# Optimization experiments

Hardware: AMD Instinct MI355X
Metric: run time of the kernel (lower is better)

The kernel has to match this reference:

```python
import jax, jax.numpy as jnp
import numpy as np

# hyperparams (match init_kwargs)
B, T, DV, DJ, L = 32, 256, 1024, 512, 20
K, S, LAYERS = 4, 2, 3
LAM = 4.0            # lambda_softmax used inside frame_by_word attention
MARGIN = 0.1         # opt.global_margin
EPS_BN = 1e-5
EPS_COS = 1e-8


def _bn(x):
    # training-mode BatchNorm1d(affine=False): per-channel stats over (batch, length)
    m = x.mean(axis=(0, 2), keepdims=True)
    v = ((x - m) ** 2).mean(axis=(0, 2), keepdims=True)
    return (x - m) / jnp.sqrt(v + EPS_BN)


def _conv1d(x, w, b, stride):
    # x: [N, Cin, L], w: [Cout, Cin, K], padding=0
    y = jax.lax.conv_general_dilated(x, w, (stride,), 'VALID',
                                     dimension_numbers=('NCH', 'OIH', 'NCH'))
    return y + b[None, :, None]


def setup_inputs() -> dict:
    key = jax.random.key(0)
    ks = jax.random.split(key, 10)
    inp = {
        'video': jax.random.normal(ks[0], (B, T, DV), jnp.float32),
        'words': jax.random.normal(ks[1], (B, L, DJ), jnp.float32),
        'w_masks': jnp.ones((B, L), jnp.float32),
        'conv0_w': jax.random.normal(ks[2], (DJ, DV, K), jnp.float32) * 0.02,
        'conv0_b': jnp.zeros((DJ,), jnp.float32),
        'conv1_w': jax.random.normal(ks[3], (DJ, DJ, K), jnp.float32) * 0.02,
        'conv1_b': jnp.zeros((DJ,), jnp.float32),
        'conv2_w': jax.random.normal(ks[4], (DJ, DJ, K), jnp.float32) * 0.02,
        'conv2_b': jnp.zeros((DJ,), jnp.float32),
        'conv1d_w': jax.random.normal(ks[5], (DJ, DJ, 1), jnp.float32) * 0.02,
        'conv1d_b': jnp.zeros((DJ,), jnp.float32),
    }
    return inp


def reference(video, words, w_masks, conv0_w, conv0_b, conv1_w, conv1_b,
              conv2_w, conv2_b, conv1d_w, conv1d_b):
    # --- conv/batchnorm feature extraction ---
    x = _bn(video.transpose(0, 2, 1))                     # [b, DV, T]
    feats = []
    for w_, b_ in ((conv0_w, conv0_b), (conv1_w, conv1_b), (conv2_w, conv2_b)):
        x = jax.nn.relu(_conv1d(x, w_, b_, S))
        feats.append(x)
    v = jnp.concatenate(feats, axis=-1)                   # [b, DJ, T']
    v = _conv1d(v, conv1d_w, conv1d_b, 1)
    v = _bn(v).transpose(0, 2, 1)                         # [b, T', DJ]
    w = _bn(words.transpose(0, 2, 1)).transpose(0, 2, 1)  # [b, L, DJ]

    # --- batched frame-by-word cross-attention over all (sentence i, video j) pairs ---
    att = jnp.einsum('jtd,ild->ijtl', v, w) * LAM         # [b_i, b_j, T', L]
    mask = (w_masks > 0.5)[:, None, None, :]
    att = jax.nn.softmax(jnp.where(mask, att, -1e9), axis=-1)
    v_s = jnp.einsum('ijtl,ild->ijtd', att, w)            # [b_i, b_j, T', DJ]

    # cosine similarity along feature dim
    num = jnp.einsum('jtd,ijtd->ijt', v, v_s)
    vn = jnp.maximum(jnp.linalg.norm(v, axis=-1), EPS_COS)[None]     # [1, b_j, T']
    vsn = jnp.maximum(jnp.linalg.norm(v_s, axis=-1), EPS_COS)        # [b_i, b_j, T']
    sim = num / (vn * vsn)                                # [b_i, b_j, T']

    b = sim.shape[0]
    idx = jnp.arange(b)
    positive_map = sim[idx, idx]                          # [b, T']
    scores = sim.max(axis=-1)                             # [b_i, b_j]

    # --- diag margin ranking loss ---
    dg = jnp.diagonal(scores)
    cost_s = jnp.clip(MARGIN + scores - dg[:, None], 0.0)
    cost_im = jnp.clip(MARGIN + scores - dg[None, :], 0.0)
    I = jnp.eye(b, dtype=bool)
    cost_s = jnp.where(I, 0.0, cost_s)
    cost_im = jnp.where(I, 0.0, cost_im)
    loss = cost_s.sum() / b + cost_im.sum() / b
    return loss, positive_map
```

## Files before the change

### kernel.cpp

```cpp
#include <hip/hip_runtime.h>
#include <math.h>

#define B_   32
#define T_   256
#define DV_  1024
#define DJ_  512
#define L_   20
#define T0_  127
#define T1_  62
#define T2_  30
#define TP_  219
#define LAM_ 4.0f
#define MARGIN_ 0.1f

typedef __attribute__((ext_vector_type(8))) short short8;
typedef __attribute__((ext_vector_type(4))) float f32x4;

static __device__ __forceinline__ unsigned short f2bf(float f) {
  union { float f; unsigned u; } v; v.f = f;
  unsigned r = v.u + 0x7fff + ((v.u >> 16) & 1);
  return (unsigned short)(r >> 16);
}

struct ushort4_t { unsigned short x, y, z, w; };

#define GLOAD_LDS16(gp, lp)                                                      \
  __builtin_amdgcn_global_load_lds(                                              \
      (const __attribute__((address_space(1))) void*)(gp),                       \
      (__attribute__((address_space(3))) void*)(lp), 16, 0, 0)

__global__ void reorder_all_k(const float* __restrict__ c0w, const float* __restrict__ c1w,
                              const float* __restrict__ c2w, const float* __restrict__ pww,
                              unsigned short* __restrict__ W0, unsigned short* __restrict__ W1,
                              unsigned short* __restrict__ W2, unsigned short* __restrict__ Wp) {
  int bid = blockIdx.x;
  if (bid < 2048) {
    int idx = bid * 256 + threadIdx.x;
    int co = idx >> 10, ci = idx & 1023;
    float4 w = *reinterpret_cast<const float4*>(c0w + (size_t)idx * 4);
    unsigned short* d = W0 + (size_t)co * 4096 + ci;
    d[0] = f2bf(w.x); d[1024] = f2bf(w.y); d[2048] = f2bf(w.z); d[3072] = f2bf(w.w);
  } else if (bid < 3072) {
    int idx = (bid - 2048) * 256 + threadIdx.x;
    int co = idx >> 9, ci = idx & 511;
    float4 w = *reinterpret_cast<const float4*>(c1w + (size_t)idx * 4);
    unsigned short* d = W1 + (size_t)co * 2048 + ci;
    d[0] = f2bf(w.x); d[512] = f2bf(w.y); d[1024] = f2bf(w.z); d[1536] = f2bf(w.w);
  } else if (bid < 4096) {
    int idx = (bid - 3072) * 256 + threadIdx.x;
    int co = idx >> 9, ci = idx & 511;
    float4 w = *reinterpret_cast<const float4*>(c2w + (size_t)idx * 4);
    unsigned short* d = W2 + (size_t)co * 2048 + ci;
    d[0] = f2bf(w.x); d[512] = f2bf(w.y); d[1024] = f2bf(w.z); d[1536] = f2bf(w.w);
  } else {
    int idx = (bid - 4096) * 256 + threadIdx.x;
    float4 v = *reinterpret_cast<const float4*>(pww + (size_t)idx * 4);
    ushort4_t h = { f2bf(v.x), f2bf(v.y), f2bf(v.z), f2bf(v.w) };
    reinterpret_cast<ushort4_t*>(Wp)[idx] = h;
  }
}

__global__ void stats1_k(const float* __restrict__ x, float* __restrict__ part,
                         int C, int rows, int rpg, int cpgShift) {
  int cpg  = 1 << cpgShift;
  int c4   = threadIdx.x & (cpg - 1);
  int rsub = threadIdx.x >> cpgShift;
  int nsub = 256 >> cpgShift;
  int r0 = blockIdx.x * rpg + rsub;
  int r1 = min(blockIdx.x * rpg + rpg, rows);
  float4 s = {0.f,0.f,0.f,0.f}, q = {0.f,0.f,0.f,0.f};
  for (int r = r0; r < r1; r += nsub) {
    float4 v = *reinterpret_cast<const float4*>(&x[(size_t)r * C + c4 * 4]);
    s.x += v.x; s.y += v.y; s.z += v.z; s.w += v.w;
    q.x += v.x*v.x; q.y += v.y*v.y; q.z += v.z*v.z; q.w += v.w*v.w;
  }
  float* ps = part + ((size_t)blockIdx.x * nsub + rsub) * 2 * C;
  reinterpret_cast<float4*>(ps)[c4] = s;
  reinterpret_cast<float4*>(ps + C)[c4] = q;
}

__global__ void stats2_k(const float* __restrict__ part, float* __restrict__ ms,
                         int C, int ng, float inv_n) {
  __shared__ float4 sS[8][33], sQ[8][33];
  int c4l = threadIdx.x & 31;
  int gs  = threadIdx.x >> 5;
  int c4  = blockIdx.x * 32 + c4l;
  float4 s = {0.f,0.f,0.f,0.f}, q = {0.f,0.f,0.f,0.f};
  for (int g = gs; g < ng; g += 8) {
    const float4* ps = reinterpret_cast<const float4*>(part + (size_t)g * 2 * C);
    float4 a = ps[c4];
    float4 b = ps[(C >> 2) + c4];
    s.x += a.x; s.y += a.y; s.z += a.z; s.w += a.w;
    q.x += b.x; q.y += b.y; q.z += b.z; q.w += b.w;
  }
  sS[gs][c4l] = s; sQ[gs][c4l] = q;
  __syncthreads();
  if (gs == 0) {
    float4 S = sS[0][c4l], Q = sQ[0][c4l];
#pragma unroll
    for (int k = 1; k < 8; ++k) {
      float4 a = sS[k][c4l], b = sQ[k][c4l];
      S.x += a.x; S.y += a.y; S.z += a.z; S.w += a.w;
      Q.x += b.x; Q.y += b.y; Q.z += b.z; Q.w += b.w;
    }
    int c = c4 * 4;
    float m0 = S.x * inv_n, m1 = S.y * inv_n, m2 = S.z * inv_n, m3 = S.w * inv_n;
    ms[c+0] = m0; ms[C+c+0] = rsqrtf(Q.x * inv_n - m0*m0 + 1e-5f);
    ms[c+1] = m1; ms[C+c+1] = rsqrtf(Q.y * inv_n - m1*m1 + 1e-5f);
    ms[c+2] = m2; ms[C+c+2] = rsqrtf(Q.z * inv_n - m2*m2 + 1e-5f);
    ms[c+3] = m3; ms[C+c+3] = rsqrtf(Q.w * inv_n - m3*m3 + 1e-5f);
  }
}

__global__ void vid_bn_cast_k(const float* __restrict__ video,
                              const float* __restrict__ ms,
                              unsigned short* __restrict__ vbf) {
  int i4 = blockIdx.x * 256 + threadIdx.x;
  float4 v = reinterpret_cast<const float4*>(video)[i4];
  int c = (i4 & 255) * 4;
  v.x = (v.x - ms[c+0]) * ms[1024+c+0];
  v.y = (v.y - ms[c+1]) * ms[1024+c+1];
  v.z = (v.z - ms[c+2]) * ms[1024+c+2];
  v.w = (v.w - ms[c+3]) * ms[1024+c+3];
  ushort4_t h = { f2bf(v.x), f2bf(v.y), f2bf(v.z), f2bf(v.w) };
  reinterpret_cast<ushort4_t*>(vbf)[i4] = h;
}

template<bool RELU, bool BIAS, bool OUT_BF16, bool PARTIAL>
__global__ __launch_bounds__(256) void mfma_gemm_k(
    const unsigned short* __restrict__ xin, const unsigned short* __restrict__ Wr,
    const float* __restrict__ bias, void* __restrict__ out,
    int b_stride, int row_off, int row_t_stride,
    int To, int M, int t_off_out, int ldout, int Ktot, int Kloc)
{
  __shared__ __align__(16) short As[2][128 * 32];
  __shared__ __align__(16) short Bs[2][128 * 32];

  const int tid  = threadIdx.x;
  const int lane = tid & 63;
  const int wv   = tid >> 6;
  const int wr   = wv >> 1;
  const int wc   = wv & 1;
  const int mbase = blockIdx.x * 128;
  const int nbase = blockIdx.y * 128;
  const int kstart = PARTIAL ? blockIdx.z * Kloc : 0;

  const int srow = tid >> 2;
  const int sb   = (((tid & 3) ^ ((srow ^ (srow >> 2)) & 3))) * 8;
  int ma0 = min(mbase + srow,      M - 1);
  int ma1 = min(mbase + 64 + srow, M - 1);
  int ba0 = ma0 / To, ta0 = ma0 % To;
  int ba1 = ma1 / To, ta1 = ma1 % To;
  const unsigned short* agp0 = xin + (size_t)ba0 * b_stride + row_off
                               + (size_t)ta0 * row_t_stride + sb + kstart;
  const unsigned short* agp1 = xin + (size_t)ba1 * b_stride + row_off
                               + (size_t)ta1 * row_t_stride + sb + kstart;
  const unsigned short* bgp0 = Wr + (size_t)(nbase + srow) * Ktot + sb + kstart;
  const unsigned short* bgp1 = Wr + (size_t)(nbase + 64 + srow) * Ktot + sb + kstart;

  f32x4 acc[4][4] = {};
  const int nsteps = Kloc >> 5;

#define STAGE(buf, k0)                                        \
  do {                                                        \
    GLOAD_LDS16(agp0 + (k0), &As[buf][wv * 512]);             \
    GLOAD_LDS16(agp1 + (k0), &As[buf][2048 + wv * 512]);      \
    GLOAD_LDS16(bgp0 + (k0), &Bs[buf][wv * 512]);             \
    GLOAD_LDS16(bgp1 + (k0), &Bs[buf][2048 + wv * 512]);      \
  } while (0)

  STAGE(0, 0);
  __syncthreads();

  const int l15   = lane & 15;
  const int rsw   = (l15 ^ (l15 >> 2)) & 3;
  const int chunk = ((lane >> 4) ^ rsw) * 8;
  const int a_off = (wr * 64 + l15) * 32 + chunk;
  const int b_off = (wc * 64 + l15) * 32 + chunk;

  for (int s = 0; s < nsteps; ++s) {
    const int nb = s & 1;
    if (s + 1 < nsteps) STAGE(nb ^ 1, (s + 1) * 32);

    const short* Ab = &As[nb][a_off];
    const short* Bb = &Bs[nb][b_off];
    short8 af[4], bf[4];
#pragma unroll
    for (int f = 0; f < 4; ++f) {
      af[f] = *reinterpret_cast<const short8*>(Ab + f * 512);
      bf[f] = *reinterpret_cast<const short8*>(Bb + f * 512);
    }
#pragma unroll
    for (int fm = 0; fm < 4; ++fm)
#pragma unroll
      for (int fn = 0; fn < 4; ++fn)
        acc[fm][fn] = __builtin_amdgcn_mfma_f32_16x16x32_bf16(af[fm], bf[fn], acc[fm][fn], 0, 0, 0);

    __syncthreads();
  }
#undef STAGE

  const int cl = lane & 15, rh = lane >> 4;
#pragma unroll
  for (int fm = 0; fm < 4; ++fm) {
#pragma unroll
    for (int fn = 0; fn < 4; ++fn) {
      int col = nbase + wc * 64 + fn * 16 + cl;
      float bv = BIAS ? bias[col] : 0.f;
      f32x4 v = acc[fm][fn];
#pragma unroll
      for (int r = 0; r < 4; ++r) {
        int m = mbase + wr * 64 + fm * 16 + rh * 4 + r;
        if (m < M) {
          if (PARTIAL) {
            float* pout = (float*)out + (size_t)blockIdx.z * ((size_t)M * ldout);
            pout[(size_t)m * ldout + col] = v[r];
          } else {
            int b = m / To, to = m % To;
            float x = v[r] + bv;
            if (RELU) x = fmaxf(x, 0.f);
            size_t oi = ((size_t)b * TP_ + t_off_out + to) * (size_t)ldout + col;
            if (OUT_BF16) ((unsigned short*)out)[oi] = f2bf(x);
            else          ((float*)out)[oi] = x;
          }
        }
      }
    }
  }
}

template<int S>
__global__ void reduce_conv_k(const float* __restrict__ part, const float* __restrict__ bias,
                              unsigned short* __restrict__ outb,
                              int M, int To, int t_off_out) {
  int idx = blockIdx.x * 256 + threadIdx.x;
  int m = idx >> 7, n4 = idx & 127;
  if (m >= M) return;
  size_t off = (size_t)m * 512 + n4 * 4;
  float4 a = *reinterpret_cast<const float4*>(part + off);
#pragma unroll
  for (int s = 1; s < S; ++s) {
    float4 b = *reinterpret_cast<const float4*>(part + (size_t)s * M * 512 + off);
    a.x += b.x; a.y += b.y; a.z += b.z; a.w += b.w;
  }
  float4 bv = *reinterpret_cast<const float4*>(bias + n4 * 4);
  a.x = fmaxf(a.x + bv.x, 0.f);
  a.y = fmaxf(a.y + bv.y, 0.f);
  a.z = fmaxf(a.z + bv.z, 0.f);
  a.w = fmaxf(a.w + bv.w, 0.f);
  int b_ = m / To, to = m % To;
  ushort4_t h = { f2bf(a.x), f2bf(a.y), f2bf(a.z), f2bf(a.w) };
  reinterpret_cast<ushort4_t*>(outb + ((size_t)b_ * TP_ + t_off_out + to) * 512)[n4] = h;
}

__global__ void v2_norm_vn_k(float* __restrict__ v2, const float* __restrict__ ms,
                             unsigned short* __restrict__ v2bf, float* __restrict__ vn) {
  int r = blockIdx.x, t = threadIdx.x;
  float* row = v2 + (size_t)r * DJ_;
  unsigned short* brow = v2bf + (size_t)r * DJ_;
  float ss = 0.f;
#pragma unroll
  for (int h = 0; h < 2; ++h) {
    int c4 = t + h * 64;
    float4 v = reinterpret_cast<float4*>(row)[c4];
    int c = c4 * 4;
    v.x = (v.x - ms[c+0]) * ms[DJ_+c+0];
    v.y = (v.y - ms[c+1]) * ms[DJ_+c+1];
    v.z = (v.z - ms[c+2]) * ms[DJ_+c+2];
    v.w = (v.w - ms[c+3]) * ms[DJ_+c+3];
    reinterpret_cast<float4*>(row)[c4] = v;
    ushort4_t h4 = { f2bf(v.x), f2bf(v.y), f2bf(v.z), f2bf(v.w) };
    reinterpret_cast<ushort4_t*>(brow)[c4] = h4;
    ss += v.x*v.x + v.y*v.y + v.z*v.z + v.w*v.w;
  }
#pragma unroll
  for (int o = 32; o; o >>= 1) ss += __shfl_down(ss, o, 64);
  if (t == 0) vn[r] = sqrtf(ss);
}

__global__ void wnorm_k(const float* __restrict__ words, const float* __restrict__ ms,
                        float* __restrict__ wbn, unsigned short* __restrict__ wbnb) {
  int idx = blockIdx.x * 256 + threadIdx.x;
  if (idx >= (B_ * L_ * DJ_) / 4) return;
  int c = (idx & 127) * 4;
  float4 v = reinterpret_cast<const float4*>(words)[idx];
  v.x = (v.x - ms[c+0]) * ms[DJ_+c+0];
  v.y = (v.y - ms[c+1]) * ms[DJ_+c+1];
  v.z = (v.z - ms[c+2]) * ms[DJ_+c+2];
  v.w = (v.w - ms[c+3]) * ms[DJ_+c+3];
  reinterpret_cast<float4*>(wbn)[idx] = v;
  ushort4_t h = { f2bf(v.x), f2bf(v.y), f2bf(v.z), f2bf(v.w) };
  reinterpret_cast<ushort4_t*>(wbnb)[idx] = h;
}

__global__ void gram_k(const float* __restrict__ wbn, float* __restrict__ G) {
  __shared__ float sw[L_ * 516];
  int i = blockIdx.x, tid = threadIdx.x;
  for (int idx = tid; idx < L_ * DJ_; idx += 256) {
    int l = idx >> 9, d = idx & 511;
    sw[l * 516 + d] = wbn[(size_t)i * L_ * DJ_ + idx];
  }
  __syncthreads();
  for (int p = tid; p < L_ * L_; p += 256) {
    int l = p / L_, l2 = p % L_;
    const float4* a = reinterpret_cast<const float4*>(&sw[l * 516]);
    const float4* b = reinterpret_cast<const float4*>(&sw[l2 * 516]);
    float acc = 0.f;
    for (int d4 = 0; d4 < 128; ++d4) {
      float4 av = a[d4], bv = b[d4];
      acc += av.x*bv.x + av.y*bv.y + av.z*bv.z + av.w*bv.w;
    }
    G[i * 400 + p] = acc;
  }
}

__global__ __launch_bounds__(256) void sim_k(
    const float* __restrict__ A, const float* __restrict__ G,
    const float* __restrict__ vn, const float* __restrict__ wmask,
    float* __restrict__ pos, float* __restrict__ scores) {
  int j = blockIdx.x, i = blockIdx.y;
  __shared__ float sG[400];
  __shared__ float sm[20];
  __shared__ float red[4];
  int tid = threadIdx.x;
  for (int p = tid; p < 400; p += 256) sG[p] = G[i * 400 + p];
  if (tid < 20) sm[tid] = wmask[i * 20 + tid];
  __syncthreads();

  float simv = -1e30f;
  if (tid < TP_) {
    const float* ar = A + ((size_t)j * TP_ + tid) * 640 + i * 20;
    float a[20], p[20];
    float mx = -1e30f;
#pragma unroll
    for (int l = 0; l < 20; ++l) {
      a[l] = ar[l];
      float lg = (sm[l] > 0.5f) ? LAM_ * a[l] : -1e9f;
      p[l] = lg;
      mx = fmaxf(mx, lg);
    }
    float Z = 0.f;
#pragma unroll
    for (int l = 0; l < 20; ++l) { p[l] = __expf(p[l] - mx); Z += p[l]; }
    float invZ = 1.f / Z, num = 0.f;
#pragma unroll
    for (int l = 0; l < 20; ++l) { p[l] *= invZ; num += p[l] * a[l]; }
    float q2 = 0.f;
#pragma unroll
    for (int l = 0; l < 20; ++l) {
      float gi = 0.f;
#pragma unroll
      for (int l2 = 0; l2 < 20; ++l2) gi += sG[l * 20 + l2] * p[l2];
      q2 += p[l] * gi;
    }
    float vnv = fmaxf(vn[(size_t)j * TP_ + tid], 1e-8f);
    float vsnv = fmaxf(sqrtf(q2), 1e-8f);
    simv = num / (vnv * vsnv);
    if (i == j) pos[i * TP_ + tid] = simv;
  }
  float mv = simv;
#pragma unroll
  for (int o = 32; o; o >>= 1) mv = fmaxf(mv, __shfl_down(mv, o, 64));
  if ((tid & 63) == 0) red[tid >> 6] = mv;
  __syncthreads();
  if (tid == 0)
    scores[i * 32 + j] = fmaxf(fmaxf(red[0], red[1]), fmaxf(red[2], red[3]));
}

__global__ void loss_k(const float* __restrict__ scores, float* __restrict__ out) {
  __shared__ float red[16];
  int tid = threadIdx.x;
  int i = tid >> 5, j = tid & 31;
  float s = scores[tid];
  float dgi = scores[i * 32 + i], dgj = scores[j * 32 + j];
  float c = 0.f;
  if (i != j)
    c = fmaxf(0.f, MARGIN_ + s - dgi) + fmaxf(0.f, MARGIN_ + s - dgj);
#pragma unroll
  for (int o = 32; o; o >>= 1) c += __shfl_down(c, o, 64);
  if ((tid & 63) == 0) red[tid >> 6] = c;
  __syncthreads();
  if (tid == 0) {
    float t = 0.f;
    for (int w = 0; w < 16; ++w) t += red[w];
    out[0] = t / 32.f;
  }
}

extern "C" void kernel_launch(void* const* d_in, const int* in_sizes, int n_in,
                              void* d_out, int out_size, void* d_ws, size_t ws_size,
                              hipStream_t stream) {
  const float* video = (const float*)d_in[0];
  const float* words = (const float*)d_in[1];
  const float* wmask = (const float*)d_in[2];
  const float* c0w = (const float*)d_in[3];
  const float* c0b = (const float*)d_in[4];
  const float* c1w = (const float*)d_in[5];
  const float* c1b = (const float*)d_in[6];
  const float* c2w = (const float*)d_in[7];
  const float* c2b = (const float*)d_in[8];
  const float* pww = (const float*)d_in[9];
  const float* pwb = (const float*)d_in[10];
  float* out = (float*)d_out;
  float* ws  = (float*)d_ws;

  float*          W0r    = ws;
  float*          W1r    = W0r + 1048576;
  float*          W2r    = W1r + 524288;
  float*          Wpw    = W2r + 524288;
  float*          AMvbf  = Wpw + 131072;
  float*          vcatb  = AMvbf + 4485120;
  float*          Pbuf   = vcatb + 1794048;
  float*          v2     = Pbuf;
  float*          v2bfp  = v2 + 3588096;
  float*          wbn    = v2bfp + 1794048;
  float*          wbnbp  = wbn + 327680;
  float*          G      = wbnbp + 163840;
  float*          vn     = G + 12800;
  float*          scores = vn + 7008;
  float*          vpart  = scores + 1024;
  float*          vms    = vpart + 1048576;
  float*          v2part = vms + 2048;
  float*          v2ms   = v2part + 897024;
  float*          wpart  = v2ms + 1024;
  float*          wms    = wpart + 81920;

  unsigned short* W0     = (unsigned short*)W0r;
  unsigned short* W1     = (unsigned short*)W1r;
  unsigned short* W2     = (unsigned short*)W2r;
  unsigned short* Wp     = (unsigned short*)Wpw;
  unsigned short* vbf    = (unsigned short*)AMvbf;
  float*          Amat   = AMvbf;
  unsigned short* vcb    = (unsigned short*)vcatb;
  unsigned short* v2bf   = (unsigned short*)v2bfp;
  unsigned short* wbnb   = (unsigned short*)wbnbp;

  reorder_all_k<<<4352, 256, 0, stream>>>(c0w, c1w, c2w, pww, W0, W1, W2, Wp);

  stats1_k<<<512, 256, 0, stream>>>(video, vpart, 1024, 8192, 16, 8);
  stats2_k<<<8, 256, 0, stream>>>(vpart, vms, 1024, 512, 1.f / 8192.f);
  vid_bn_cast_k<<<8192, 256, 0, stream>>>(video, vms, vbf);

  mfma_gemm_k<false, false, false, true><<<dim3(32, 4, 4), 256, 0, stream>>>(
      vbf, W0, nullptr, Pbuf, 262144, 0, 2048, T0_, 32 * T0_, 0, 512, 4096, 1024);
  reduce_conv_k<4><<<2032, 256, 0, stream>>>(Pbuf, c0b, vcb, 32 * T0_, T0_, 0);
  mfma_gemm_k<false, false, false, true><<<dim3(16, 4, 8), 256, 0, stream>>>(
      vcb, W1, nullptr, Pbuf, 112128, 0, 1024, T1_, 32 * T1_, 0, 512, 2048, 256);
  reduce_conv_k<8><<<992, 256, 0, stream>>>(Pbuf, c1b, vcb, 32 * T1_, T1_, T0_);
  mfma_gemm_k<false, false, false, true><<<dim3(8, 4, 8), 256, 0, stream>>>(
      vcb, W2, nullptr, Pbuf, 112128, 65024, 1024, T2_, 32 * T2_, 0, 512, 2048, 256);
  reduce_conv_k<8><<<480, 256, 0, stream>>>(Pbuf, c2b, vcb, 32 * T2_, T2_, T0_ + T1_);

  mfma_gemm_k<false, true, false, false><<<dim3(55, 4), 256, 0, stream>>>(
      vcb, Wp, pwb, v2, 112128, 0, 512, TP_, 32 * TP_, 0, 512, 512, 512);

  stats1_k<<<438, 256, 0, stream>>>(v2, v2part, 512, 7008, 16, 7);
  stats2_k<<<4, 256, 0, stream>>>(v2part, v2ms, 512, 876, 1.f / 7008.f);
  v2_norm_vn_k<<<7008, 64, 0, stream>>>(v2, v2ms, v2bf, vn);

  stats1_k<<<40, 256, 0, stream>>>(words, wpart, 512, 640, 16, 7);
  stats2_k<<<4, 256, 0, stream>>>(wpart, wms, 512, 80, 1.f / 640.f);
  wnorm_k<<<(81920 + 255) / 256, 256, 0, stream>>>(words, wms, wbn, wbnb);
  gram_k<<<32, 256, 0, stream>>>(wbn, G);

  mfma_gemm_k<false, false, false, false><<<dim3(55, 5), 256, 0, stream>>>(
      v2bf, wbnb, nullptr, Amat, 112128, 0, 512, TP_, 32 * TP_, 0, 640, 512, 512);

  sim_k<<<dim3(32, 32), 256, 0, stream>>>(Amat, G, vn, wmask, out + 1, scores);
  loss_k<<<1, 1024, 0, stream>>>(scores, out);
}
```

Before: 246.5 us.

## Template GEMM tile sizes and remap workgroups across XCDs

Turns the MFMA GEMM into a template over the block tile (BM, BN). The conv and projection GEMMs now launch with smaller 64x128 or 64x64 tiles, giving more workgroups to fill the 256 CUs. It also adds a linear workgroup remapping so consecutive tiles land on the same XCD, aiming to improve L2 reuse. Smaller tiles lower per-block arithmetic intensity and raise global and LDS traffic per FLOP.

```diff
diff --git a/kernel.cpp b/kernel.cpp
--- a/kernel.cpp
+++ b/kernel.cpp
@@ -126,47 +126,64 @@
   reinterpret_cast<ushort4_t*>(vbf)[i4] = h;
 }
 
-template<bool RELU, bool BIAS, bool OUT_BF16, bool PARTIAL>
-__global__ __launch_bounds__(256) void mfma_gemm_k(
+template<int BM, int BN, bool RELU, bool BIAS, bool OUT_BF16, bool PARTIAL>
+__global__ __launch_bounds__(256) void gemm_k(
     const unsigned short* __restrict__ xin, const unsigned short* __restrict__ Wr,
     const float* __restrict__ bias, void* __restrict__ out,
     int b_stride, int row_off, int row_t_stride,
     int To, int M, int t_off_out, int ldout, int Ktot, int Kloc)
 {
-  __shared__ __align__(16) short As[2][128 * 32];
-  __shared__ __align__(16) short Bs[2][128 * 32];
+  constexpr int AI = BM / 64, BI = BN / 64;
+  constexpr int FM = BM / 32, FN = BN / 32;
+  __shared__ __align__(16) short As[2][BM * 32];
+  __shared__ __align__(16) short Bs[2][BN * 32];
 
   const int tid  = threadIdx.x;
   const int lane = tid & 63;
   const int wv   = tid >> 6;
   const int wr   = wv >> 1;
   const int wc   = wv & 1;
-  const int mbase = blockIdx.x * 128;
-  const int nbase = blockIdx.y * 128;
-  const int kstart = PARTIAL ? blockIdx.z * Kloc : 0;
+
+  const int gx = gridDim.x, gy = gridDim.y;
+  const int nwg = gx * gy * gridDim.z;
+  const int lin = blockIdx.x + gx * (blockIdx.y + gy * blockIdx.z);
+  const int q = nwg >> 3, r = nwg & 7;
+  const int xcd = lin & 7, sub = lin >> 3;
+  const int work = (xcd < r ? xcd * (q + 1) : r * (q + 1) + (xcd - r) * q) + sub;
+  const int bx = work % gx;
+  const int by = (work / gx) % gy;
+  const int bz = work / (gx * gy);
+
+  const int mbase = bx * BM;
+  const int nbase = by * BN;
+  const int kstart = PARTIAL ? bz * Kloc : 0;
 
   const int srow = tid >> 2;
   const int sb   = (((tid & 3) ^ ((srow ^ (srow >> 2)) & 3))) * 8;
-  int ma0 = min(mbase + srow,      M - 1);
-  int ma1 = min(mbase + 64 + srow, M - 1);
-  int ba0 = ma0 / To, ta0 = ma0 % To;
-  int ba1 = ma1 / To, ta1 = ma1 % To;
-  const unsigned short* agp0 = xin + (size_t)ba0 * b_stride + row_off
-                               + (size_t)ta0 * row_t_stride + sb + kstart;
-  const unsigned short* agp1 = xin + (size_t)ba1 * b_stride + row_off
-                               + (size_t)ta1 * row_t_stride + sb + kstart;
-  const unsigned short* bgp0 = Wr + (size_t)(nbase + srow) * Ktot + sb + kstart;
-  const unsigned short* bgp1 = Wr + (size_t)(nbase + 64 + srow) * Ktot + sb + kstart;
-
-  f32x4 acc[4][4] = {};
+  const unsigned short* agp[AI];
+  const unsigned short* bgp[BI];
+#pragma unroll
+  for (int i = 0; i < AI; ++i) {
+    int ma = min(mbase + i * 64 + srow, M - 1);
+    int b0 = ma / To, t0 = ma % To;
+    agp[i] = xin + (size_t)b0 * b_stride + row_off
+             + (size_t)t0 * row_t_stride + sb + kstart;
+  }
+#pragma unroll
+  for (int i = 0; i < BI; ++i)
+    bgp[i] = Wr + (size_t)(nbase + i * 64 + srow) * Ktot + sb + kstart;
+
+  f32x4 acc[FM][FN] = {};
   const int nsteps = Kloc >> 5;
 
-#define STAGE(buf, k0)                                        \
-  do {                                                        \
-    GLOAD_LDS16(agp0 + (k0), &As[buf][wv * 512]);             \
-    GLOAD_LDS16(agp1 + (k0), &As[buf][2048 + wv * 512]);      \
-    GLOAD_LDS16(bgp0 + (k0), &Bs[buf][wv * 512]);             \
-    GLOAD_LDS16(bgp1 + (k0), &Bs[buf][2048 + wv * 512]);      \
+#define STAGE(buf, k0)                                                \
+  do {                                                                \
+    _Pragma("unroll")                                                 \
+    for (int i = 0; i < AI; ++i)                                      \
+      GLOAD_LDS16(agp[i] + (k0), &As[buf][i * 2048 + wv * 512]);      \
+    _Pragma("unroll")                                                 \
+    for (int i = 0; i < BI; ++i)                                      \
+      GLOAD_LDS16(bgp[i] + (k0), &Bs[buf][i * 2048 + wv * 512]);      \
   } while (0)
 
   STAGE(0, 0);
@@ -175,8 +192,8 @@
   const int l15   = lane & 15;
   const int rsw   = (l15 ^ (l15 >> 2)) & 3;
   const int chunk = ((lane >> 4) ^ rsw) * 8;
-  const int a_off = (wr * 64 + l15) * 32 + chunk;
-  const int b_off = (wc * 64 + l15) * 32 + chunk;
+  const int a_off = (wr * (BM / 2) + l15) * 32 + chunk;
+  const int b_off = (wc * (BN / 2) + l15) * 32 + chunk;
 
   for (int s = 0; s < nsteps; ++s) {
     const int nb = s & 1;
@@ -184,16 +201,17 @@
 
     const short* Ab = &As[nb][a_off];
     const short* Bb = &Bs[nb][b_off];
-    short8 af[4], bf[4];
-#pragma unroll
-    for (int f = 0; f < 4; ++f) {
+    short8 af[FM], bf[FN];
+#pragma unroll
+    for (int f = 0; f < FM; ++f)
       af[f] = *reinterpret_cast<const short8*>(Ab + f * 512);
+#pragma unroll
+    for (int f = 0; f < FN; ++f)
       bf[f] = *reinterpret_cast<const short8*>(Bb + f * 512);
-    }
-#pragma unroll
-    for (int fm = 0; fm < 4; ++fm)
-#pragma unroll
-      for (int fn = 0; fn < 4; ++fn)
+#pragma unroll
+    for (int fm = 0; fm < FM; ++fm)
+#pragma unroll
+      for (int fn = 0; fn < FN; ++fn)
         acc[fm][fn] = __builtin_amdgcn_mfma_f32_16x16x32_bf16(af[fm], bf[fn], acc[fm][fn], 0, 0, 0);
 
     __syncthreads();
@@ -202,22 +220,22 @@
 
   const int cl = lane & 15, rh = lane >> 4;
 #pragma unroll
-  for (int fm = 0; fm < 4; ++fm) {
-#pragma unroll
-    for (int fn = 0; fn < 4; ++fn) {
-      int col = nbase + wc * 64 + fn * 16 + cl;
+  for (int fm = 0; fm < FM; ++fm) {
+#pragma unroll
+    for (int fn = 0; fn < FN; ++fn) {
+      int col = nbase + wc * (BN / 2) + fn * 16 + cl;
       float bv = BIAS ? bias[col] : 0.f;
       f32x4 v = acc[fm][fn];
 #pragma unroll
-      for (int r = 0; r < 4; ++r) {
-        int m = mbase + wr * 64 + fm * 16 + rh * 4 + r;
+      for (int rr = 0; rr < 4; ++rr) {
+        int m = mbase + wr * (BM / 2) + fm * 16 + rh * 4 + rr;
         if (m < M) {
           if (PARTIAL) {
-            float* pout = (float*)out + (size_t)blockIdx.z * ((size_t)M * ldout);
-            pout[(size_t)m * ldout + col] = v[r];
+            float* pout = (float*)out + (size_t)bz * ((size_t)M * ldout);
+            pout[(size_t)m * ldout + col] = v[rr];
           } else {
             int b = m / To, to = m % To;
-            float x = v[r] + bv;
+            float x = v[rr] + bv;
             if (RELU) x = fmaxf(x, 0.f);
             size_t oi = ((size_t)b * TP_ + t_off_out + to) * (size_t)ldout + col;
             if (OUT_BF16) ((unsigned short*)out)[oi] = f2bf(x);
@@ -441,17 +459,17 @@
   stats2_k<<<8, 256, 0, stream>>>(vpart, vms, 1024, 512, 1.f / 8192.f);
   vid_bn_cast_k<<<8192, 256, 0, stream>>>(video, vms, vbf);
 
-  mfma_gemm_k<false, false, false, true><<<dim3(32, 4, 4), 256, 0, stream>>>(
+  gemm_k<64, 128, false, false, false, true><<<dim3(64, 4, 4), 256, 0, stream>>>(
       vbf, W0, nullptr, Pbuf, 262144, 0, 2048, T0_, 32 * T0_, 0, 512, 4096, 1024);
   reduce_conv_k<4><<<2032, 256, 0, stream>>>(Pbuf, c0b, vcb, 32 * T0_, T0_, 0);
-  mfma_gemm_k<false, false, false, true><<<dim3(16, 4, 8), 256, 0, stream>>>(
+  gemm_k<64, 128, false, false, false, true><<<dim3(31, 4, 8), 256, 0, stream>>>(
       vcb, W1, nullptr, Pbuf, 112128, 0, 1024, T1_, 32 * T1_, 0, 512, 2048, 256);
   reduce_conv_k<8><<<992, 256, 0, stream>>>(Pbuf, c1b, vcb, 32 * T1_, T1_, T0_);
-  mfma_gemm_k<false, false, false, true><<<dim3(8, 4, 8), 256, 0, stream>>>(
+  gemm_k<64, 64, false, false, false, true><<<dim3(15, 8, 8), 256, 0, stream>>>(
       vcb, W2, nullptr, Pbuf, 112128, 65024, 1024, T2_, 32 * T2_, 0, 512, 2048, 256);
   reduce_conv_k<8><<<480, 256, 0, stream>>>(Pbuf, c2b, vcb, 32 * T2_, T2_, T0_ + T1_);
 
-  mfma_gemm_k<false, true, false, false><<<dim3(55, 4), 256, 0, stream>>>(
+  gemm_k<64, 64, false, true, false, false><<<dim3(110, 8), 256, 0, stream>>>(
       vcb, Wp, pwb, v2, 112128, 0, 512, TP_, 32 * TP_, 0, 512, 512, 512);
 
   stats1_k<<<438, 256, 0, stream>>>(v2, v2part, 512, 7008, 16, 7);
@@ -463,7 +481,7 @@
   wnorm_k<<<(81920 + 255) / 256, 256, 0, stream>>>(words, wms, wbn, wbnb);
   gram_k<<<32, 256, 0, stream>>>(wbn, G);
 
-  mfma_gemm_k<false, false, false, false><<<dim3(55, 5), 256, 0, stream>>>(
+  gemm_k<64, 64, false, false, false, false><<<dim3(110, 10), 256, 0, stream>>>(
       v2bf, wbnb, nullptr, Amat, 112128, 0, 512, TP_, 32 * TP_, 0, 640, 512, 512);
 
   sim_k<<<dim3(32, 32), 256, 0, stream>>>(Amat, G, vn, wmask, out + 1, scores);
```

New measurement: 244.3 us. Within noise of the previous version (-0.9%).
